# Optimization experiments

Hardware: AMD Instinct MI355X
Metric: run time of the kernel (lower is better)

The kernel has to match this reference:

```python
import jax, jax.numpy as jnp
import numpy as np

P = 1024          # nodes per graph
B = 64            # graphs in batch
N = P * B         # total nodes
E = N * 32        # total edges (avg degree 32)
D_IN = 16         # per-node feature dim (share_obs_dim)
H = 32            # GCN / MLP hidden dim (hardcoded in GNet)
SHARE = 64        # flat share_state dim


def setup_inputs() -> dict:
    key = jax.random.key(0)
    ks = jax.random.split(key, 20)

    x = jax.random.normal(ks[0], (N, D_IN), jnp.float32)
    src = jax.random.randint(ks[1], (E,), 0, N, dtype=jnp.int32)
    # keep edges inside each 1024-node graph block (PyG batched graphs)
    dst = (src // P) * P + jax.random.randint(ks[2], (E,), 0, P, dtype=jnp.int32)
    edge_index = jnp.stack([src, dst])
    value_batch = (jnp.arange(N, dtype=jnp.int32) // P)
    share_state = jax.random.normal(ks[3], (B, SHARE), jnp.float32)

    def lin(k, o, i):
        return jax.random.normal(k, (o, i), jnp.float32) / np.float32(np.sqrt(i))

    return {
        "x": x, "edge_index": edge_index, "value_batch": value_batch,
        "share_state": share_state,
        # value_gnet: GCNConv(D_IN,32), GCNConv(32,32), Linear(32,32), post-pool Linear(32,32)
        "W1": lin(ks[4], H, D_IN), "b1": jnp.zeros((H,), jnp.float32),
        "W2": lin(ks[5], H, H),    "b2": jnp.zeros((H,), jnp.float32),
        "Wl": lin(ks[6], H, H),    "bl": jnp.zeros((H,), jnp.float32),
        "Wp": lin(ks[7], H, H),    "bp": jnp.zeros((H,), jnp.float32),
        # value_net MLP: SHARE->32->32->32
        "Vw1": lin(ks[8], H, SHARE), "Vb1": jnp.zeros((H,), jnp.float32),
        "Vw2": lin(ks[9], H, H),     "Vb2": jnp.zeros((H,), jnp.float32),
        "Vw3": lin(ks[10], H, H),    "Vb3": jnp.zeros((H,), jnp.float32),
        # value_comnet: 64->32->1
        "Cw1": lin(ks[11], H, 2 * H), "Cb1": jnp.zeros((H,), jnp.float32),
        "Cw2": lin(ks[12], 1, H) * np.float32(0.01), "Cb2": jnp.zeros((1,), jnp.float32),
    }


def gcn_conv(x, src, dst, W, b):
    """PyG GCNConv: D^-1/2 (A+I) D^-1/2 X W^T + b (unit edge weights)."""
    n = x.shape[0]
    loop = jnp.arange(n, dtype=src.dtype)
    s = jnp.concatenate([src, loop])
    d = jnp.concatenate([dst, loop])
    deg = jax.ops.segment_sum(jnp.ones(s.shape[0], x.dtype), d, num_segments=n)
    dis = jnp.where(deg > 0, jax.lax.rsqrt(jnp.maximum(deg, 1e-12)), 0.0)
    norm = dis[s] * dis[d]                      # [E+N]
    h = x @ W.T                                  # [N, H] small GEMM first
    out = jax.ops.segment_sum(h[s] * norm[:, None], d, num_segments=n)
    return out + b


def reference(x, edge_index, value_batch, share_state,
              W1, b1, W2, b2, Wl, bl, Wp, bp,
              Vw1, Vb1, Vw2, Vb2, Vw3, Vb3,
              Cw1, Cb1, Cw2, Cb2):
    src, dst = edge_index[0], edge_index[1]
    nb = share_state.shape[0]

    # value_gnet
    h = jnp.tanh(gcn_conv(x, src, dst, W1, b1))
    h = jnp.tanh(gcn_conv(h, src, dst, W2, b2))
    h = jnp.tanh(h @ Wl.T + bl)
    pooled = jax.ops.segment_sum(h, value_batch, num_segments=nb)  # global_add_pool -> [B, 32]
    h1 = pooled @ Wp.T + bp

    # value_net MLP on flat share_state
    h2 = jnp.tanh(share_state @ Vw1.T + Vb1)
    h2 = jnp.tanh(h2 @ Vw2.T + Vb2)
    h2 = h2 @ Vw3.T + Vb3

    # value_comnet
    z = jnp.tanh(jnp.concatenate([h1, h2], axis=-1) @ Cw1.T + Cb1)
    value = z @ Cw2.T + Cb2                      # [B, 1]
    return value
```

## Files before the change

kernel.cpp:

```cpp
#include <hip/hip_runtime.h>
#include <math.h>

#define NEDGES 2097152
#define CAPB   9216
#define CAPQ   9728

#define OFF_GFILL 0u
#define OFF_CTR   1024u
#define OFF_ARR1  1152u
#define OFF_ARR2  1408u
#define OFF_ARR3  1664u
#define OFF_POOL4 2048u
#define OFF_DIS   34816u
#define OFF_H1G   296960u
#define OFF_EBUF  8685568u

__device__ __forceinline__ float ftanh(float x) {
    float e = __expf(2.f * x);
    return 1.f - 2.f * __builtin_amdgcn_rcpf(e + 1.f);
}

__global__ __launch_bounds__(1024, 1) void k_main(
        const float* __restrict__ x,
        const int* __restrict__ src, const int* __restrict__ dst,
        const float* __restrict__ W1, const float* __restrict__ b1,
        const float* __restrict__ W2, const float* __restrict__ b2,
        const float* __restrict__ Wl, const float* __restrict__ bl,
        const float* __restrict__ Wp, const float* __restrict__ bp,
        const float* __restrict__ Vw1, const float* __restrict__ Vb1,
        const float* __restrict__ Vw2, const float* __restrict__ Vb2,
        const float* __restrict__ Vw3, const float* __restrict__ Vb3,
        const float* __restrict__ Cw1, const float* __restrict__ Cb1,
        const float* __restrict__ Cw2, const float* __restrict__ Cb2,
        const float* __restrict__ share,
        int* __restrict__ gfill, int* __restrict__ ctr,
        int* __restrict__ arr1, int* __restrict__ arr2, int* __restrict__ arr3,
        unsigned int* __restrict__ ebuf, float* __restrict__ disg,
        float* __restrict__ h1g, float* __restrict__ pooled4,
        float* __restrict__ out) {
    __shared__ float hsL[1025 * 32];
    __shared__ unsigned short lcsr[CAPQ];
    __shared__ int hist[256], lrow[256], lfill[256], gbase[256];
    __shared__ int wsum[4];
    float4* hsL4 = (float4*)hsL;
    unsigned int* sorted = (unsigned int*)hsL;

    int t = threadIdx.x;
    int blk = blockIdx.x;
    int lane = t & 63, wid = t >> 6;

    if (t < 256) { hist[t] = 0; lfill[t] = 0; }
    __syncthreads();

    unsigned int pk[8];
    {
        const int4* s4p = (const int4*)(src + blk * 8192);
        const int4* d4p = (const int4*)(dst + blk * 8192);
        #pragma unroll
        for (int k = 0; k < 2; k++) {
            int4 s4 = s4p[k * 1024 + t];
            int4 d4 = d4p[k * 1024 + t];
            int ss[4] = { s4.x, s4.y, s4.z, s4.w };
            int dd[4] = { d4.x, d4.y, d4.z, d4.w };
            #pragma unroll
            for (int j = 0; j < 4; j++) {
                int gg = ss[j] >> 10;
                pk[k * 4 + j] = (unsigned int)((ss[j] & 1023) | ((dd[j] & 1023) << 10) | (gg << 20));
                atomicAdd(&hist[(gg << 2) | ((dd[j] >> 8) & 3)], 1);
            }
        }
    }
    __syncthreads();

    int hA = 0, xxA = 0;
    if (t < 256) {
        hA = hist[t];
        xxA = hA;
        #pragma unroll
        for (int off = 1; off < 64; off <<= 1) {
            int y = __shfl_up(xxA, off, 64);
            if (lane >= off) xxA += y;
        }
        if (lane == 63) wsum[wid] = xxA;
    }
    __syncthreads();
    if (t < 256) {
        int pre = 0;
        for (int w = 0; w < wid; w++) pre += wsum[w];
        lrow[t] = pre + xxA - hA;
        gbase[t] = atomicAdd(&gfill[t], hA);
    }
    __syncthreads();

    #pragma unroll
    for (int k = 0; k < 8; k++) {
        int b = pk[k] >> 18;
        int pos = lrow[b] + atomicAdd(&lfill[b], 1);
        sorted[pos] = pk[k];
    }
    __syncthreads();
    #pragma unroll
    for (int k = 0; k < 8; k++) {
        int i = k * 1024 + t;
        unsigned int p = sorted[i];
        int b = p >> 18;
        ebuf[(size_t)b * CAPB + gbase[b] + (i - lrow[b])] = p;
    }
    __syncthreads();
    if (t == 0)
        __hip_atomic_fetch_add(ctr, 1, __ATOMIC_RELEASE, __HIP_MEMORY_SCOPE_AGENT);

    int g = blk & 63, part = blk >> 6;

    float inr[16];
    {
        const float4* in4 = (const float4*)(x + ((size_t)((g << 10) + t)) * 16);
        #pragma unroll
        for (int k = 0; k < 4; k++) {
            float4 v = in4[k];
            inr[4*k] = v.x; inr[4*k+1] = v.y; inr[4*k+2] = v.z; inr[4*k+3] = v.w;
        }
    }
    if (t == 0) {
        while (__hip_atomic_load(ctr, __ATOMIC_RELAXED, __HIP_MEMORY_SCOPE_AGENT) < 256) {}
        (void)__hip_atomic_load(ctr, __ATOMIC_ACQUIRE, __HIP_MEMORY_SCOPE_AGENT);
    }
    __syncthreads();

    int bkt = (g << 2) | part;
    int cnt = gfill[bkt];
    const unsigned int* eb = ebuf + (size_t)bkt * CAPB;

    if (t < 256) hist[t] = 0;
    if (t < 32) hsL[1024 * 32 + t] = 0.f;
    __syncthreads();

    for (int i = t; i < cnt; i += 1024) atomicAdd(&hist[(eb[i] >> 10) & 255], 1);
    __syncthreads();

    int dq = 0, r4 = 0;
    if (t < 256) {
        dq = hist[t]; r4 = (dq + 3) & ~3;
        disg[(g << 10) + part * 256 + t] = rsqrtf((float)(dq + 1));
    }
    __syncthreads();
    if (t == 0)
        __hip_atomic_fetch_add(arr1 + g, 1, __ATOMIC_RELEASE, __HIP_MEMORY_SCOPE_AGENT);

    int xx = r4;
    #pragma unroll
    for (int off = 1; off < 64; off <<= 1) {
        int y = __shfl_up(xx, off, 64);
        if (lane >= off) xx += y;
    }
    if (t < 256 && lane == 63) wsum[wid] = xx;
    __syncthreads();
    if (t < 256) {
        int pre = 0;
        for (int w = 0; w < wid; w++) pre += wsum[w];
        lrow[t] = pre + xx - r4;
        lfill[t] = 0;
    }
    __syncthreads();

    for (int i = t; i < cnt; i += 1024) {
        unsigned int v = eb[i];
        int dl = (v >> 10) & 255;
        int pos = lrow[dl] + atomicAdd(&lfill[dl], 1);
        lcsr[pos] = (unsigned short)(v & 1023);
    }
    if (t < 256) {
        int st = lrow[t];
        for (int i = dq; i < r4; i++) lcsr[st + i] = 1024;
    }

    if (t == 0) {
        while (__hip_atomic_load(arr1 + g, __ATOMIC_RELAXED, __HIP_MEMORY_SCOPE_AGENT) < 4) {}
        (void)__hip_atomic_load(arr1 + g, __ATOMIC_ACQUIRE, __HIP_MEMORY_SCOPE_AGENT);
    }
    __syncthreads();

    float dis_t = disg[(g << 10) + t];
    int sw = t & 7;

    #pragma unroll
    for (int o4 = 0; o4 < 8; o4++) {
        float r[4];
        #pragma unroll
        for (int j = 0; j < 4; j++) {
            int o = o4 * 4 + j;
            float s = 0.f;
            #pragma unroll
            for (int k = 0; k < 16; k++) s += inr[k] * W1[o * 16 + k];
            r[j] = s * dis_t;
        }
        hsL4[t * 8 + (o4 ^ sw)] = make_float4(r[0], r[1], r[2], r[3]);
    }
    __syncthreads();

    int q = t & 7, grp = t >> 3;
    #pragma unroll
    for (int pass = 0; pass < 2; pass++) {
        int lq = pass * 128 + grp;
        int ln = part * 256 + lq;
        int d = hist[lq];
        float dn = rsqrtf((float)(d + 1));
        int st = lrow[lq];
        float4 acc = hsL4[ln * 8 + (q ^ (ln & 7))];
        const ushort4* c4 = (const ushort4*)(lcsr + st);
        int d4 = (d + 3) >> 2;
        for (int i = 0; i < d4; i++) {
            ushort4 ss = c4[i];
            float4 v0 = hsL4[ss.x * 8 + (q ^ (ss.x & 7))];
            float4 v1 = hsL4[ss.y * 8 + (q ^ (ss.y & 7))];
            float4 v2 = hsL4[ss.z * 8 + (q ^ (ss.z & 7))];
            float4 v3 = hsL4[ss.w * 8 + (q ^ (ss.w & 7))];
            acc.x += (v0.x + v1.x) + (v2.x + v3.x);
            acc.y += (v0.y + v1.y) + (v2.y + v3.y);
            acc.z += (v0.z + v1.z) + (v2.z + v3.z);
            acc.w += (v0.w + v1.w) + (v2.w + v3.w);
        }
        float4 bb = ((const float4*)b1)[q];
        float4 r;
        r.x = ftanh(dn * acc.x + bb.x);
        r.y = ftanh(dn * acc.y + bb.y);
        r.z = ftanh(dn * acc.z + bb.z);
        r.w = ftanh(dn * acc.w + bb.w);
        ((float4*)h1g)[((size_t)(g << 10) + ln) * 8 + q] = r;
    }
    __syncthreads();
    if (t == 0) {
        __hip_atomic_fetch_add(arr2 + g, 1, __ATOMIC_RELEASE, __HIP_MEMORY_SCOPE_AGENT);
        while (__hip_atomic_load(arr2 + g, __ATOMIC_RELAXED, __HIP_MEMORY_SCOPE_AGENT) < 4) {}
        (void)__hip_atomic_load(arr2 + g, __ATOMIC_ACQUIRE, __HIP_MEMORY_SCOPE_AGENT);
    }
    __syncthreads();

    float r2[32];
    {
        const float4* h4 = (const float4*)(h1g + ((size_t)(g << 10) + t) * 32);
        #pragma unroll
        for (int k = 0; k < 8; k++) {
            float4 v = h4[k];
            r2[4*k] = v.x; r2[4*k+1] = v.y; r2[4*k+2] = v.z; r2[4*k+3] = v.w;
        }
    }
    #pragma unroll
    for (int o4 = 0; o4 < 8; o4++) {
        float r[4];
        #pragma unroll
        for (int j = 0; j < 4; j++) {
            int o = o4 * 4 + j;
            float s = 0.f;
            #pragma unroll
            for (int k = 0; k < 32; k++) s += r2[k] * W2[o * 32 + k];
            r[j] = s * dis_t;
        }
        hsL4[t * 8 + (o4 ^ sw)] = make_float4(r[0], r[1], r[2], r[3]);
    }
    __syncthreads();

    float4 racc[2];
    #pragma unroll
    for (int pass = 0; pass < 2; pass++) {
        int lq = pass * 128 + grp;
        int ln = part * 256 + lq;
        int d = hist[lq];
        float dn = rsqrtf((float)(d + 1));
        int st = lrow[lq];
        float4 acc = hsL4[ln * 8 + (q ^ (ln & 7))];
        const ushort4* c4 = (const ushort4*)(lcsr + st);
        int d4 = (d + 3) >> 2;
        for (int i = 0; i < d4; i++) {
            ushort4 ss = c4[i];
            float4 v0 = hsL4[ss.x * 8 + (q ^ (ss.x & 7))];
            float4 v1 = hsL4[ss.y * 8 + (q ^ (ss.y & 7))];
            float4 v2 = hsL4[ss.z * 8 + (q ^ (ss.z & 7))];
            float4 v3 = hsL4[ss.w * 8 + (q ^ (ss.w & 7))];
            acc.x += (v0.x + v1.x) + (v2.x + v3.x);
            acc.y += (v0.y + v1.y) + (v2.y + v3.y);
            acc.z += (v0.z + v1.z) + (v2.z + v3.z);
            acc.w += (v0.w + v1.w) + (v2.w + v3.w);
        }
        float4 bb = ((const float4*)b2)[q];
        float4 r;
        r.x = ftanh(dn * acc.x + bb.x);
        r.y = ftanh(dn * acc.y + bb.y);
        r.z = ftanh(dn * acc.z + bb.z);
        r.w = ftanh(dn * acc.w + bb.w);
        racc[pass] = r;
    }

    __syncthreads();
    #pragma unroll
    for (int pass = 0; pass < 2; pass++) {
        int lnn = pass * 128 + grp;
        hsL4[lnn * 8 + (q ^ (lnn & 7))] = racc[pass];
    }
    __syncthreads();
    int o = t & 31, seg = t >> 5;
    float ps = 0.f;
    {
        float wlr[32];
        #pragma unroll
        for (int k = 0; k < 32; k++) wlr[k] = Wl[o * 32 + k];
        float blv = bl[o];
        #pragma unroll
        for (int j = 0; j < 8; j++) {
            int nl = seg * 8 + j;
            int swn = nl & 7;
            float s = blv;
            #pragma unroll
            for (int k = 0; k < 32; k++) {
                float h2v = hsL[nl * 32 + ((((k >> 2) ^ swn) << 2) | (k & 3))];
                s += h2v * wlr[k];
            }
            ps += ftanh(s);
        }
    }
    float* psum = hsL + 8192;
    psum[t] = ps;
    __syncthreads();
    if (t < 32) {
        float tot = 0.f;
        for (int s2 = 0; s2 < 32; s2++) tot += psum[s2 * 32 + t];
        pooled4[(g * 4 + part) * 32 + t] = tot;
    }

    __syncthreads();
    if (t == 0)
        __hip_atomic_fetch_add(arr3 + g, 1, __ATOMIC_RELEASE, __HIP_MEMORY_SCOPE_AGENT);
    if (part == 0) {
        if (t == 0) {
            while (__hip_atomic_load(arr3 + g, __ATOMIC_RELAXED, __HIP_MEMORY_SCOPE_AGENT) < 4) {}
            (void)__hip_atomic_load(arr3 + g, __ATOMIC_ACQUIRE, __HIP_MEMORY_SCOPE_AGENT);
        }
        __syncthreads();
        if (t < 32) {
            int j = t;
            float p = pooled4[(g * 4 + 0) * 32 + j] + pooled4[(g * 4 + 1) * 32 + j]
                    + pooled4[(g * 4 + 2) * 32 + j] + pooled4[(g * 4 + 3) * 32 + j];
            float h1v = bp[j];
            #pragma unroll
            for (int k = 0; k < 32; k++) h1v += Wp[j * 32 + k] * __shfl(p, k, 32);
            float s0 = share[g * 64 + j];
            float s1 = share[g * 64 + 32 + j];
            float t1 = Vb1[j];
            #pragma unroll
            for (int k = 0; k < 32; k++) {
                t1 += Vw1[j * 64 + k] * __shfl(s0, k, 32);
                t1 += Vw1[j * 64 + 32 + k] * __shfl(s1, k, 32);
            }
            t1 = tanhf(t1);
            float t2 = Vb2[j];
            #pragma unroll
            for (int k = 0; k < 32; k++) t2 += Vw2[j * 32 + k] * __shfl(t1, k, 32);
            t2 = tanhf(t2);
            float h2v = Vb3[j];
            #pragma unroll
            for (int k = 0; k < 32; k++) h2v += Vw3[j * 32 + k] * __shfl(t2, k, 32);
            float z = Cb1[j];
            #pragma unroll
            for (int k = 0; k < 32; k++) {
                z += Cw1[j * 64 + k] * __shfl(h1v, k, 32);
                z += Cw1[j * 64 + 32 + k] * __shfl(h2v, k, 32);
            }
            z = tanhf(z);
            float v = Cw2[j] * z;
            v += __shfl_down(v, 16, 32); v += __shfl_down(v, 8, 32);
            v += __shfl_down(v, 4, 32);  v += __shfl_down(v, 2, 32);
            v += __shfl_down(v, 1, 32);
            if (j == 0) out[g] = v + Cb2[0];
        }
    }
}

extern "C" void kernel_launch(void* const* d_in, const int* in_sizes, int n_in,
                              void* d_out, int out_size, void* d_ws, size_t ws_size,
                              hipStream_t stream) {
    const float* x     = (const float*)d_in[0];
    const int*   ei    = (const int*)d_in[1];
    const float* share = (const float*)d_in[3];
    const float* W1 = (const float*)d_in[4];  const float* b1 = (const float*)d_in[5];
    const float* W2 = (const float*)d_in[6];  const float* b2 = (const float*)d_in[7];
    const float* Wl = (const float*)d_in[8];  const float* bl = (const float*)d_in[9];
    const float* Wp = (const float*)d_in[10]; const float* bp = (const float*)d_in[11];
    const float* Vw1 = (const float*)d_in[12]; const float* Vb1 = (const float*)d_in[13];
    const float* Vw2 = (const float*)d_in[14]; const float* Vb2 = (const float*)d_in[15];
    const float* Vw3 = (const float*)d_in[16]; const float* Vb3 = (const float*)d_in[17];
    const float* Cw1 = (const float*)d_in[18]; const float* Cb1 = (const float*)d_in[19];
    const float* Cw2 = (const float*)d_in[20]; const float* Cb2 = (const float*)d_in[21];

    char* ws = (char*)d_ws;
    int*          gfill   = (int*)(ws + OFF_GFILL);
    int*          ctr     = (int*)(ws + OFF_CTR);
    int*          arr1    = (int*)(ws + OFF_ARR1);
    int*          arr2    = (int*)(ws + OFF_ARR2);
    int*          arr3    = (int*)(ws + OFF_ARR3);
    float*        pooled4 = (float*)(ws + OFF_POOL4);
    float*        disg    = (float*)(ws + OFF_DIS);
    float*        h1g     = (float*)(ws + OFF_H1G);
    unsigned int* ebuf    = (unsigned int*)(ws + OFF_EBUF);

    const int* srcp = ei;
    const int* dstp = ei + NEDGES;

    hipMemsetAsync(ws, 0, 2048, stream);

    k_main<<<256, 1024, 0, stream>>>(x, srcp, dstp,
                                     W1, b1, W2, b2, Wl, bl, Wp, bp,
                                     Vw1, Vb1, Vw2, Vb2, Vw3, Vb3,
                                     Cw1, Cb1, Cw2, Cb2, share,
                                     gfill, ctr, arr1, arr2, arr3,
                                     ebuf, disg, h1g, pooled4, (float*)d_out);
}
```

Baseline: 205.0 us.

## Split edge bucketing into separate kernel and store node features as fp16 in LDS

The single fused kernel is split into a bucketing kernel and a GCN kernel, which replaces the grid-wide spin barrier on a global counter with a kernel boundary. Per-node transformed features in shared memory are now stored as packed half precision. This halves the LDS footprint and the gather bandwidth during neighbor aggregation. The trade-off is an extra kernel launch, the need to reload state, and reduced precision in the aggregated features.

```diff
diff --git a/kernel.cpp b/kernel.cpp
--- a/kernel.cpp
+++ b/kernel.cpp
@@ -1,4 +1,5 @@
 #include <hip/hip_runtime.h>
+#include <hip/hip_fp16.h>
 #include <math.h>
 
 #define NEDGES 2097152
@@ -6,10 +7,9 @@
 #define CAPQ   9728
 
 #define OFF_GFILL 0u
-#define OFF_CTR   1024u
-#define OFF_ARR1  1152u
-#define OFF_ARR2  1408u
-#define OFF_ARR3  1664u
+#define OFF_ARR1  1024u
+#define OFF_ARR2  1280u
+#define OFF_ARR3  1536u
 #define OFF_POOL4 2048u
 #define OFF_DIS   34816u
 #define OFF_H1G   296960u
@@ -20,9 +20,89 @@
     return 1.f - 2.f * __builtin_amdgcn_rcpf(e + 1.f);
 }
 
-__global__ __launch_bounds__(1024, 1) void k_main(
+__device__ __forceinline__ float4 ld4h(const unsigned int* hs, int r, int q) {
+    uint2 u = *(const uint2*)(hs + r * 16 + ((q ^ (r & 7)) << 1));
+    float2 fa = __half22float2(*(const __half2*)&u.x);
+    float2 fb = __half22float2(*(const __half2*)&u.y);
+    return make_float4(fa.x, fa.y, fb.x, fb.y);
+}
+__device__ __forceinline__ uint2 pk4h(float a, float b, float c, float d) {
+    __half2 h0 = __floats2half2_rn(a, b);
+    __half2 h1 = __floats2half2_rn(c, d);
+    return make_uint2(*(unsigned int*)&h0, *(unsigned int*)&h1);
+}
+
+__global__ __launch_bounds__(1024) void k_bucket(
+        const int* __restrict__ src, const int* __restrict__ dst,
+        int* __restrict__ gfill, unsigned int* __restrict__ ebuf) {
+    __shared__ unsigned int sorted[8192];
+    __shared__ int hist[256], lexcl[256], gbase[256], lfill[256];
+    __shared__ int wsum[4];
+    int t = threadIdx.x;
+    int blk = blockIdx.x;
+    int lane = t & 63, wid = t >> 6;
+
+    if (t < 256) { hist[t] = 0; lfill[t] = 0; }
+    __syncthreads();
+
+    unsigned int pk[8];
+    {
+        const int4* s4p = (const int4*)(src + blk * 8192);
+        const int4* d4p = (const int4*)(dst + blk * 8192);
+        #pragma unroll
+        for (int k = 0; k < 2; k++) {
+            int4 s4 = s4p[k * 1024 + t];
+            int4 d4 = d4p[k * 1024 + t];
+            int ss[4] = { s4.x, s4.y, s4.z, s4.w };
+            int dd[4] = { d4.x, d4.y, d4.z, d4.w };
+            #pragma unroll
+            for (int j = 0; j < 4; j++) {
+                int gg = ss[j] >> 10;
+                pk[k * 4 + j] = (unsigned int)((ss[j] & 1023) | ((dd[j] & 1023) << 10) | (gg << 20));
+                atomicAdd(&hist[(gg << 2) | ((dd[j] >> 8) & 3)], 1);
+            }
+        }
+    }
+    __syncthreads();
+
+    int hA = 0, xxA = 0;
+    if (t < 256) {
+        hA = hist[t];
+        xxA = hA;
+        #pragma unroll
+        for (int off = 1; off < 64; off <<= 1) {
+            int y = __shfl_up(xxA, off, 64);
+            if (lane >= off) xxA += y;
+        }
+        if (lane == 63) wsum[wid] = xxA;
+    }
+    __syncthreads();
+    if (t < 256) {
+        int pre = 0;
+        for (int w = 0; w < wid; w++) pre += wsum[w];
+        lexcl[t] = pre + xxA - hA;
+        gbase[t] = atomicAdd(&gfill[t], hA);
+    }
+    __syncthreads();
+
+    #pragma unroll
+    for (int k = 0; k < 8; k++) {
+        int b = pk[k] >> 18;
+        int pos = lexcl[b] + atomicAdd(&lfill[b], 1);
+        sorted[pos] = pk[k];
+    }
+    __syncthreads();
+    #pragma unroll
+    for (int k = 0; k < 8; k++) {
+        int i = k * 1024 + t;
+        unsigned int p = sorted[i];
+        int b = p >> 18;
+        ebuf[(size_t)b * CAPB + gbase[b] + (i - lexcl[b])] = p;
+    }
+}
+
+__global__ __launch_bounds__(1024, 1) void k_gcn(
         const float* __restrict__ x,
-        const int* __restrict__ src, const int* __restrict__ dst,
         const float* __restrict__ W1, const float* __restrict__ b1,
         const float* __restrict__ W2, const float* __restrict__ b2,
         const float* __restrict__ Wl, const float* __restrict__ bl,
@@ -33,106 +113,34 @@
         const float* __restrict__ Cw1, const float* __restrict__ Cb1,
         const float* __restrict__ Cw2, const float* __restrict__ Cb2,
         const float* __restrict__ share,
-        int* __restrict__ gfill, int* __restrict__ ctr,
+        const unsigned int* __restrict__ ebuf, const int* __restrict__ gfill,
+        float* __restrict__ disg, float* __restrict__ h1g,
         int* __restrict__ arr1, int* __restrict__ arr2, int* __restrict__ arr3,
-        unsigned int* __restrict__ ebuf, float* __restrict__ disg,
-        float* __restrict__ h1g, float* __restrict__ pooled4,
-        float* __restrict__ out) {
-    __shared__ float hsL[1025 * 32];
-    __shared__ unsigned short lcsr[CAPQ];
-    __shared__ int hist[256], lrow[256], lfill[256], gbase[256];
+        float* __restrict__ pooled4, float* __restrict__ out) {
+    __shared__ unsigned int hsLh[1025 * 16];
+    __shared__ __align__(16) unsigned short lcsr[CAPQ];
+    __shared__ int hist[256], lrow[256], lfill[256];
     __shared__ int wsum[4];
-    float4* hsL4 = (float4*)hsL;
-    unsigned int* sorted = (unsigned int*)hsL;
 
     int t = threadIdx.x;
-    int blk = blockIdx.x;
+    int g = blockIdx.x & 63, part = blockIdx.x >> 6;
+    int bkt = (g << 2) | part;
+    int cnt = gfill[bkt];
+    const unsigned int* eb = ebuf + (size_t)bkt * CAPB;
     int lane = t & 63, wid = t >> 6;
-
-    if (t < 256) { hist[t] = 0; lfill[t] = 0; }
-    __syncthreads();
-
-    unsigned int pk[8];
-    {
-        const int4* s4p = (const int4*)(src + blk * 8192);
-        const int4* d4p = (const int4*)(dst + blk * 8192);
-        #pragma unroll
-        for (int k = 0; k < 2; k++) {
-            int4 s4 = s4p[k * 1024 + t];
-            int4 d4 = d4p[k * 1024 + t];
-            int ss[4] = { s4.x, s4.y, s4.z, s4.w };
-            int dd[4] = { d4.x, d4.y, d4.z, d4.w };
-            #pragma unroll
-            for (int j = 0; j < 4; j++) {
-                int gg = ss[j] >> 10;
-                pk[k * 4 + j] = (unsigned int)((ss[j] & 1023) | ((dd[j] & 1023) << 10) | (gg << 20));
-                atomicAdd(&hist[(gg << 2) | ((dd[j] >> 8) & 3)], 1);
-            }
-        }
-    }
-    __syncthreads();
-
-    int hA = 0, xxA = 0;
-    if (t < 256) {
-        hA = hist[t];
-        xxA = hA;
-        #pragma unroll
-        for (int off = 1; off < 64; off <<= 1) {
-            int y = __shfl_up(xxA, off, 64);
-            if (lane >= off) xxA += y;
-        }
-        if (lane == 63) wsum[wid] = xxA;
-    }
-    __syncthreads();
-    if (t < 256) {
-        int pre = 0;
-        for (int w = 0; w < wid; w++) pre += wsum[w];
-        lrow[t] = pre + xxA - hA;
-        gbase[t] = atomicAdd(&gfill[t], hA);
-    }
-    __syncthreads();
-
-    #pragma unroll
-    for (int k = 0; k < 8; k++) {
-        int b = pk[k] >> 18;
-        int pos = lrow[b] + atomicAdd(&lfill[b], 1);
-        sorted[pos] = pk[k];
-    }
-    __syncthreads();
-    #pragma unroll
-    for (int k = 0; k < 8; k++) {
-        int i = k * 1024 + t;
-        unsigned int p = sorted[i];
-        int b = p >> 18;
-        ebuf[(size_t)b * CAPB + gbase[b] + (i - lrow[b])] = p;
-    }
-    __syncthreads();
-    if (t == 0)
-        __hip_atomic_fetch_add(ctr, 1, __ATOMIC_RELEASE, __HIP_MEMORY_SCOPE_AGENT);
-
-    int g = blk & 63, part = blk >> 6;
 
     float inr[16];
     {
-        const float4* in4 = (const float4*)(x + ((size_t)((g << 10) + t)) * 16);
+        const float4* in4 = (const float4*)(x + ((size_t)(g << 10) + t) * 16);
         #pragma unroll
         for (int k = 0; k < 4; k++) {
             float4 v = in4[k];
             inr[4*k] = v.x; inr[4*k+1] = v.y; inr[4*k+2] = v.z; inr[4*k+3] = v.w;
         }
     }
-    if (t == 0) {
-        while (__hip_atomic_load(ctr, __ATOMIC_RELAXED, __HIP_MEMORY_SCOPE_AGENT) < 256) {}
-        (void)__hip_atomic_load(ctr, __ATOMIC_ACQUIRE, __HIP_MEMORY_SCOPE_AGENT);
-    }
-    __syncthreads();
-
-    int bkt = (g << 2) | part;
-    int cnt = gfill[bkt];
-    const unsigned int* eb = ebuf + (size_t)bkt * CAPB;
 
     if (t < 256) hist[t] = 0;
-    if (t < 32) hsL[1024 * 32 + t] = 0.f;
+    if (t < 16) hsLh[1024 * 16 + t] = 0u;
     __syncthreads();
 
     for (int i = t; i < cnt; i += 1024) atomicAdd(&hist[(eb[i] >> 10) & 255], 1);
@@ -194,7 +202,7 @@
             for (int k = 0; k < 16; k++) s += inr[k] * W1[o * 16 + k];
             r[j] = s * dis_t;
         }
-        hsL4[t * 8 + (o4 ^ sw)] = make_float4(r[0], r[1], r[2], r[3]);
+        *(uint2*)&hsLh[t * 16 + ((o4 ^ sw) << 1)] = pk4h(r[0], r[1], r[2], r[3]);
     }
     __syncthreads();
 
@@ -206,15 +214,15 @@
         int d = hist[lq];
         float dn = rsqrtf((float)(d + 1));
         int st = lrow[lq];
-        float4 acc = hsL4[ln * 8 + (q ^ (ln & 7))];
+        float4 acc = ld4h(hsLh, ln, q);
         const ushort4* c4 = (const ushort4*)(lcsr + st);
         int d4 = (d + 3) >> 2;
         for (int i = 0; i < d4; i++) {
             ushort4 ss = c4[i];
-            float4 v0 = hsL4[ss.x * 8 + (q ^ (ss.x & 7))];
-            float4 v1 = hsL4[ss.y * 8 + (q ^ (ss.y & 7))];
-            float4 v2 = hsL4[ss.z * 8 + (q ^ (ss.z & 7))];
-            float4 v3 = hsL4[ss.w * 8 + (q ^ (ss.w & 7))];
+            float4 v0 = ld4h(hsLh, ss.x, q);
+            float4 v1 = ld4h(hsLh, ss.y, q);
+            float4 v2 = ld4h(hsLh, ss.z, q);
+            float4 v3 = ld4h(hsLh, ss.w, q);
             acc.x += (v0.x + v1.x) + (v2.x + v3.x);
             acc.y += (v0.y + v1.y) + (v2.y + v3.y);
             acc.z += (v0.z + v1.z) + (v2.z + v3.z);
@@ -236,27 +244,27 @@
     }
     __syncthreads();
 
-    float r2[32];
     {
+        float r2[32];
         const float4* h4 = (const float4*)(h1g + ((size_t)(g << 10) + t) * 32);
         #pragma unroll
         for (int k = 0; k < 8; k++) {
             float4 v = h4[k];
             r2[4*k] = v.x; r2[4*k+1] = v.y; r2[4*k+2] = v.z; r2[4*k+3] = v.w;
         }
-    }
-    #pragma unroll
-    for (int o4 = 0; o4 < 8; o4++) {
-        float r[4];
-        #pragma unroll
-        for (int j = 0; j < 4; j++) {
-            int o = o4 * 4 + j;
-            float s = 0.f;
-            #pragma unroll
-            for (int k = 0; k < 32; k++) s += r2[k] * W2[o * 32 + k];
-            r[j] = s * dis_t;
-        }
-        hsL4[t * 8 + (o4 ^ sw)] = make_float4(r[0], r[1], r[2], r[3]);
+        #pragma unroll
+        for (int o4 = 0; o4 < 8; o4++) {
+            float r[4];
+            #pragma unroll
+            for (int j = 0; j < 4; j++) {
+                int o = o4 * 4 + j;
+                float s = 0.f;
+                #pragma unroll
+                for (int k = 0; k < 32; k++) s += r2[k] * W2[o * 32 + k];
+                r[j] = s * dis_t;
+            }
+            *(uint2*)&hsLh[t * 16 + ((o4 ^ sw) << 1)] = pk4h(r[0], r[1], r[2], r[3]);
+        }
     }
     __syncthreads();
 
@@ -268,15 +276,15 @@
         int d = hist[lq];
         float dn = rsqrtf((float)(d + 1));
         int st = lrow[lq];
-        float4 acc = hsL4[ln * 8 + (q ^ (ln & 7))];
+        float4 acc = ld4h(hsLh, ln, q);
         const ushort4* c4 = (const ushort4*)(lcsr + st);
         int d4 = (d + 3) >> 2;
         for (int i = 0; i < d4; i++) {
             ushort4 ss = c4[i];
-            float4 v0 = hsL4[ss.x * 8 + (q ^ (ss.x & 7))];
-            float4 v1 = hsL4[ss.y * 8 + (q ^ (ss.y & 7))];
-            float4 v2 = hsL4[ss.z * 8 + (q ^ (ss.z & 7))];
-            float4 v3 = hsL4[ss.w * 8 + (q ^ (ss.w & 7))];
+            float4 v0 = ld4h(hsLh, ss.x, q);
+            float4 v1 = ld4h(hsLh, ss.y, q);
+            float4 v2 = ld4h(hsLh, ss.z, q);
+            float4 v3 = ld4h(hsLh, ss.w, q);
             acc.x += (v0.x + v1.x) + (v2.x + v3.x);
             acc.y += (v0.y + v1.y) + (v2.y + v3.y);
             acc.z += (v0.z + v1.z) + (v2.z + v3.z);
@@ -290,14 +298,16 @@
         r.w = ftanh(dn * acc.w + bb.w);
         racc[pass] = r;
     }
-
-    __syncthreads();
+    __syncthreads();
+
     #pragma unroll
     for (int pass = 0; pass < 2; pass++) {
-        int lnn = pass * 128 + grp;
-        hsL4[lnn * 8 + (q ^ (lnn & 7))] = racc[pass];
-    }
-    __syncthreads();
+        int ln = part * 256 + pass * 128 + grp;
+        *(uint2*)&hsLh[ln * 16 + ((q ^ (ln & 7)) << 1)] =
+            pk4h(racc[pass].x, racc[pass].y, racc[pass].z, racc[pass].w);
+    }
+    __syncthreads();
+
     int o = t & 31, seg = t >> 5;
     float ps = 0.f;
     {
@@ -307,18 +317,17 @@
         float blv = bl[o];
         #pragma unroll
         for (int j = 0; j < 8; j++) {
-            int nl = seg * 8 + j;
-            int swn = nl & 7;
+            int row = part * 256 + seg * 8 + j;
             float s = blv;
             #pragma unroll
-            for (int k = 0; k < 32; k++) {
-                float h2v = hsL[nl * 32 + ((((k >> 2) ^ swn) << 2) | (k & 3))];
-                s += h2v * wlr[k];
+            for (int p2 = 0; p2 < 8; p2++) {
+                float4 v = ld4h(hsLh, row, p2);
+                s += v.x * wlr[4*p2] + v.y * wlr[4*p2+1] + v.z * wlr[4*p2+2] + v.w * wlr[4*p2+3];
             }
             ps += ftanh(s);
         }
     }
-    float* psum = hsL + 8192;
+    float* psum = (float*)lcsr;
     psum[t] = ps;
     __syncthreads();
     if (t < 32) {
@@ -326,10 +335,10 @@
         for (int s2 = 0; s2 < 32; s2++) tot += psum[s2 * 32 + t];
         pooled4[(g * 4 + part) * 32 + t] = tot;
     }
-
     __syncthreads();
     if (t == 0)
         __hip_atomic_fetch_add(arr3 + g, 1, __ATOMIC_RELEASE, __HIP_MEMORY_SCOPE_AGENT);
+
     if (part == 0) {
         if (t == 0) {
             while (__hip_atomic_load(arr3 + g, __ATOMIC_RELAXED, __HIP_MEMORY_SCOPE_AGENT) < 4) {}
@@ -393,7 +402,6 @@
 
     char* ws = (char*)d_ws;
     int*          gfill   = (int*)(ws + OFF_GFILL);
-    int*          ctr     = (int*)(ws + OFF_CTR);
     int*          arr1    = (int*)(ws + OFF_ARR1);
     int*          arr2    = (int*)(ws + OFF_ARR2);
     int*          arr3    = (int*)(ws + OFF_ARR3);
@@ -407,10 +415,10 @@
 
     hipMemsetAsync(ws, 0, 2048, stream);
 
-    k_main<<<256, 1024, 0, stream>>>(x, srcp, dstp,
-                                     W1, b1, W2, b2, Wl, bl, Wp, bp,
-                                     Vw1, Vb1, Vw2, Vb2, Vw3, Vb3,
-                                     Cw1, Cb1, Cw2, Cb2, share,
-                                     gfill, ctr, arr1, arr2, arr3,
-                                     ebuf, disg, h1g, pooled4, (float*)d_out);
-}
+    k_bucket<<<256, 1024, 0, stream>>>(srcp, dstp, gfill, ebuf);
+    k_gcn<<<256, 1024, 0, stream>>>(x, W1, b1, W2, b2, Wl, bl, Wp, bp,
+                                    Vw1, Vb1, Vw2, Vb2, Vw3, Vb3,
+                                    Cw1, Cb1, Cw2, Cb2, share,
+                                    ebuf, gfill, disg, h1g,
+                                    arr1, arr2, arr3, pooled4, (float*)d_out);
+}
```

After: 181.3 us. -11.6%, faster.

## Split edge bucketing into separate kernel, replacing global spin barrier

Applied to the files above, without the earlier changes.

Moves the edge-bucketing phase into its own kernel, k_bucket, which is launched before the GCN kernel. This replaces the grid-wide atomic counter spin-wait with kernel-launch ordering. The bucketing kernel no longer shares the large LDS footprint, so it may get higher occupancy. The X·W1 product is also hoisted into registers before the arr1 wait, so it overlaps the sync. The cost is an extra kernel launch and a second read of ebuf and gfill from global memory.

```diff
diff --git a/kernel.cpp b/kernel.cpp
--- a/kernel.cpp
+++ b/kernel.cpp
@@ -6,10 +6,9 @@
 #define CAPQ   9728
 
 #define OFF_GFILL 0u
-#define OFF_CTR   1024u
-#define OFF_ARR1  1152u
-#define OFF_ARR2  1408u
-#define OFF_ARR3  1664u
+#define OFF_ARR1  1024u
+#define OFF_ARR2  1280u
+#define OFF_ARR3  1536u
 #define OFF_POOL4 2048u
 #define OFF_DIS   34816u
 #define OFF_H1G   296960u
@@ -20,9 +19,77 @@
     return 1.f - 2.f * __builtin_amdgcn_rcpf(e + 1.f);
 }
 
-__global__ __launch_bounds__(1024, 1) void k_main(
+__global__ __launch_bounds__(1024) void k_bucket(
+        const int* __restrict__ src, const int* __restrict__ dst,
+        int* __restrict__ gfill, unsigned int* __restrict__ ebuf) {
+    __shared__ unsigned int sorted[8192];
+    __shared__ int hist[256], lexcl[256], gbase[256], lfill[256];
+    __shared__ int wsum[4];
+    int t = threadIdx.x;
+    int blk = blockIdx.x;
+    int lane = t & 63, wid = t >> 6;
+
+    if (t < 256) { hist[t] = 0; lfill[t] = 0; }
+    __syncthreads();
+
+    unsigned int pk[8];
+    {
+        const int4* s4p = (const int4*)(src + blk * 8192);
+        const int4* d4p = (const int4*)(dst + blk * 8192);
+        #pragma unroll
+        for (int k = 0; k < 2; k++) {
+            int4 s4 = s4p[k * 1024 + t];
+            int4 d4 = d4p[k * 1024 + t];
+            int ss[4] = { s4.x, s4.y, s4.z, s4.w };
+            int dd[4] = { d4.x, d4.y, d4.z, d4.w };
+            #pragma unroll
+            for (int j = 0; j < 4; j++) {
+                int gg = ss[j] >> 10;
+                pk[k * 4 + j] = (unsigned int)((ss[j] & 1023) | ((dd[j] & 1023) << 10) | (gg << 20));
+                atomicAdd(&hist[(gg << 2) | ((dd[j] >> 8) & 3)], 1);
+            }
+        }
+    }
+    __syncthreads();
+
+    int hA = 0, xxA = 0;
+    if (t < 256) {
+        hA = hist[t];
+        xxA = hA;
+        #pragma unroll
+        for (int off = 1; off < 64; off <<= 1) {
+            int y = __shfl_up(xxA, off, 64);
+            if (lane >= off) xxA += y;
+        }
+        if (lane == 63) wsum[wid] = xxA;
+    }
+    __syncthreads();
+    if (t < 256) {
+        int pre = 0;
+        for (int w = 0; w < wid; w++) pre += wsum[w];
+        lexcl[t] = pre + xxA - hA;
+        gbase[t] = atomicAdd(&gfill[t], hA);
+    }
+    __syncthreads();
+
+    #pragma unroll
+    for (int k = 0; k < 8; k++) {
+        int b = pk[k] >> 18;
+        int pos = lexcl[b] + atomicAdd(&lfill[b], 1);
+        sorted[pos] = pk[k];
+    }
+    __syncthreads();
+    #pragma unroll
+    for (int k = 0; k < 8; k++) {
+        int i = k * 1024 + t;
+        unsigned int p = sorted[i];
+        int b = p >> 18;
+        ebuf[(size_t)b * CAPB + gbase[b] + (i - lexcl[b])] = p;
+    }
+}
+
+__global__ __launch_bounds__(1024, 1) void k_gcn(
         const float* __restrict__ x,
-        const int* __restrict__ src, const int* __restrict__ dst,
         const float* __restrict__ W1, const float* __restrict__ b1,
         const float* __restrict__ W2, const float* __restrict__ b2,
         const float* __restrict__ Wl, const float* __restrict__ bl,
@@ -33,103 +100,32 @@
         const float* __restrict__ Cw1, const float* __restrict__ Cb1,
         const float* __restrict__ Cw2, const float* __restrict__ Cb2,
         const float* __restrict__ share,
-        int* __restrict__ gfill, int* __restrict__ ctr,
+        const unsigned int* __restrict__ ebuf, const int* __restrict__ gfill,
+        float* __restrict__ disg, float* __restrict__ h1g,
         int* __restrict__ arr1, int* __restrict__ arr2, int* __restrict__ arr3,
-        unsigned int* __restrict__ ebuf, float* __restrict__ disg,
-        float* __restrict__ h1g, float* __restrict__ pooled4,
-        float* __restrict__ out) {
+        float* __restrict__ pooled4, float* __restrict__ out) {
     __shared__ float hsL[1025 * 32];
     __shared__ unsigned short lcsr[CAPQ];
-    __shared__ int hist[256], lrow[256], lfill[256], gbase[256];
+    __shared__ int hist[256], lrow[256], lfill[256];
     __shared__ int wsum[4];
     float4* hsL4 = (float4*)hsL;
-    unsigned int* sorted = (unsigned int*)hsL;
 
     int t = threadIdx.x;
-    int blk = blockIdx.x;
+    int g = blockIdx.x & 63, part = blockIdx.x >> 6;
+    int bkt = (g << 2) | part;
+    int cnt = gfill[bkt];
+    const unsigned int* eb = ebuf + (size_t)bkt * CAPB;
     int lane = t & 63, wid = t >> 6;
-
-    if (t < 256) { hist[t] = 0; lfill[t] = 0; }
-    __syncthreads();
-
-    unsigned int pk[8];
-    {
-        const int4* s4p = (const int4*)(src + blk * 8192);
-        const int4* d4p = (const int4*)(dst + blk * 8192);
-        #pragma unroll
-        for (int k = 0; k < 2; k++) {
-            int4 s4 = s4p[k * 1024 + t];
-            int4 d4 = d4p[k * 1024 + t];
-            int ss[4] = { s4.x, s4.y, s4.z, s4.w };
-            int dd[4] = { d4.x, d4.y, d4.z, d4.w };
-            #pragma unroll
-            for (int j = 0; j < 4; j++) {
-                int gg = ss[j] >> 10;
-                pk[k * 4 + j] = (unsigned int)((ss[j] & 1023) | ((dd[j] & 1023) << 10) | (gg << 20));
-                atomicAdd(&hist[(gg << 2) | ((dd[j] >> 8) & 3)], 1);
-            }
-        }
-    }
-    __syncthreads();
-
-    int hA = 0, xxA = 0;
-    if (t < 256) {
-        hA = hist[t];
-        xxA = hA;
-        #pragma unroll
-        for (int off = 1; off < 64; off <<= 1) {
-            int y = __shfl_up(xxA, off, 64);
-            if (lane >= off) xxA += y;
-        }
-        if (lane == 63) wsum[wid] = xxA;
-    }
-    __syncthreads();
-    if (t < 256) {
-        int pre = 0;
-        for (int w = 0; w < wid; w++) pre += wsum[w];
-        lrow[t] = pre + xxA - hA;
-        gbase[t] = atomicAdd(&gfill[t], hA);
-    }
-    __syncthreads();
-
-    #pragma unroll
-    for (int k = 0; k < 8; k++) {
-        int b = pk[k] >> 18;
-        int pos = lrow[b] + atomicAdd(&lfill[b], 1);
-        sorted[pos] = pk[k];
-    }
-    __syncthreads();
-    #pragma unroll
-    for (int k = 0; k < 8; k++) {
-        int i = k * 1024 + t;
-        unsigned int p = sorted[i];
-        int b = p >> 18;
-        ebuf[(size_t)b * CAPB + gbase[b] + (i - lrow[b])] = p;
-    }
-    __syncthreads();
-    if (t == 0)
-        __hip_atomic_fetch_add(ctr, 1, __ATOMIC_RELEASE, __HIP_MEMORY_SCOPE_AGENT);
-
-    int g = blk & 63, part = blk >> 6;
 
     float inr[16];
     {
-        const float4* in4 = (const float4*)(x + ((size_t)((g << 10) + t)) * 16);
+        const float4* in4 = (const float4*)(x + ((size_t)(g << 10) + t) * 16);
         #pragma unroll
         for (int k = 0; k < 4; k++) {
             float4 v = in4[k];
             inr[4*k] = v.x; inr[4*k+1] = v.y; inr[4*k+2] = v.z; inr[4*k+3] = v.w;
         }
     }
-    if (t == 0) {
-        while (__hip_atomic_load(ctr, __ATOMIC_RELAXED, __HIP_MEMORY_SCOPE_AGENT) < 256) {}
-        (void)__hip_atomic_load(ctr, __ATOMIC_ACQUIRE, __HIP_MEMORY_SCOPE_AGENT);
-    }
-    __syncthreads();
-
-    int bkt = (g << 2) | part;
-    int cnt = gfill[bkt];
-    const unsigned int* eb = ebuf + (size_t)bkt * CAPB;
 
     if (t < 256) hist[t] = 0;
     if (t < 32) hsL[1024 * 32 + t] = 0.f;
@@ -146,6 +142,15 @@
     __syncthreads();
     if (t == 0)
         __hip_atomic_fetch_add(arr1 + g, 1, __ATOMIC_RELEASE, __HIP_MEMORY_SCOPE_AGENT);
+
+    float xw[32];
+    #pragma unroll
+    for (int o = 0; o < 32; o++) {
+        float s = 0.f;
+        #pragma unroll
+        for (int k = 0; k < 16; k++) s += inr[k] * W1[o * 16 + k];
+        xw[o] = s;
+    }
 
     int xx = r4;
     #pragma unroll
@@ -184,18 +189,9 @@
     int sw = t & 7;
 
     #pragma unroll
-    for (int o4 = 0; o4 < 8; o4++) {
-        float r[4];
-        #pragma unroll
-        for (int j = 0; j < 4; j++) {
-            int o = o4 * 4 + j;
-            float s = 0.f;
-            #pragma unroll
-            for (int k = 0; k < 16; k++) s += inr[k] * W1[o * 16 + k];
-            r[j] = s * dis_t;
-        }
-        hsL4[t * 8 + (o4 ^ sw)] = make_float4(r[0], r[1], r[2], r[3]);
-    }
+    for (int o4 = 0; o4 < 8; o4++)
+        hsL4[t * 8 + (o4 ^ sw)] = make_float4(xw[4*o4] * dis_t, xw[4*o4+1] * dis_t,
+                                              xw[4*o4+2] * dis_t, xw[4*o4+3] * dis_t);
     __syncthreads();
 
     int q = t & 7, grp = t >> 3;
@@ -326,10 +322,10 @@
         for (int s2 = 0; s2 < 32; s2++) tot += psum[s2 * 32 + t];
         pooled4[(g * 4 + part) * 32 + t] = tot;
     }
-
     __syncthreads();
     if (t == 0)
         __hip_atomic_fetch_add(arr3 + g, 1, __ATOMIC_RELEASE, __HIP_MEMORY_SCOPE_AGENT);
+
     if (part == 0) {
         if (t == 0) {
             while (__hip_atomic_load(arr3 + g, __ATOMIC_RELAXED, __HIP_MEMORY_SCOPE_AGENT) < 4) {}
@@ -393,7 +389,6 @@
 
     char* ws = (char*)d_ws;
     int*          gfill   = (int*)(ws + OFF_GFILL);
-    int*          ctr     = (int*)(ws + OFF_CTR);
     int*          arr1    = (int*)(ws + OFF_ARR1);
     int*          arr2    = (int*)(ws + OFF_ARR2);
     int*          arr3    = (int*)(ws + OFF_ARR3);
@@ -407,10 +402,10 @@
 
     hipMemsetAsync(ws, 0, 2048, stream);
 
-    k_main<<<256, 1024, 0, stream>>>(x, srcp, dstp,
-                                     W1, b1, W2, b2, Wl, bl, Wp, bp,
-                                     Vw1, Vb1, Vw2, Vb2, Vw3, Vb3,
-                                     Cw1, Cb1, Cw2, Cb2, share,
-                                     gfill, ctr, arr1, arr2, arr3,
-                                     ebuf, disg, h1g, pooled4, (float*)d_out);
+    k_bucket<<<256, 1024, 0, stream>>>(srcp, dstp, gfill, ebuf);
+    k_gcn<<<256, 1024, 0, stream>>>(x, W1, b1, W2, b2, Wl, bl, Wp, bp,
+                                    Vw1, Vb1, Vw2, Vb2, Vw3, Vb3,
+                                    Cw1, Cb1, Cw2, Cb2, share,
+                                    ebuf, gfill, disg, h1g,
+                                    arr1, arr2, arr3, pooled4, (float*)d_out);
 }
```

Measured after the change: 184.4 us. 10.0% less time.
